# Kernel optimization log

Measured on AMD Instinct MI355X. Metric: run time of the kernel, lower is better.

The kernel has to match this reference:

```python
import jax, jax.numpy as jnp
import numpy as np

B, T, D, DL, E, H, K = 4, 2048, 1024, 128, 8, 4, 3
HD = DL // H


def setup_inputs() -> dict:
    key = jax.random.key(0)
    ks = jax.random.split(key, 12)
    s = jnp.float32(0.02)
    f = lambda k, shape: jax.random.normal(k, shape, dtype=jnp.float32)
    zeros = lambda n: jnp.zeros((n,), jnp.float32)
    ones = lambda n: jnp.ones((n,), jnp.float32)
    return {
        "x": f(ks[0], (B, T, D)),
        "w_down": f(ks[1], (E * DL, D)) * s,
        "expert_pos_embed": f(ks[2], (1, E, DL)) * s,
        "global_proj_w": f(ks[3], (DL, D)) * s,
        "global_proj_b": zeros(DL),
        "attn_in_w": f(ks[4], (3 * DL, DL)) * s,
        "attn_in_b": zeros(3 * DL),
        "attn_out_w": f(ks[5], (DL, DL)) * s,
        "attn_out_b": zeros(DL),
        "norm_w": ones(DL),
        "norm_b": zeros(DL),
        "rq1_w": f(ks[6], (DL, DL)) * s,
        "rq1_b": zeros(DL),
        "rq_ln_w": ones(DL),
        "rq_ln_b": zeros(DL),
        "rq2_w": f(ks[7], (DL, DL)) * s,
        "rq2_b": zeros(DL),
        "rk_w": f(ks[8], (DL, DL)) * s,
        "rk_b": zeros(DL),
        "w_up": f(ks[9], (E, DL, D)) * s,
    }


def _ln(x, w, b):
    m = jnp.mean(x, axis=-1, keepdims=True)
    v = jnp.mean((x - m) ** 2, axis=-1, keepdims=True)
    return (x - m) * jax.lax.rsqrt(v + 1e-5) * w + b


def _gelu(x):
    return jax.nn.gelu(x, approximate=False)  # torch nn.GELU() default is exact erf


def reference(x, w_down, expert_pos_embed, global_proj_w, global_proj_b,
              attn_in_w, attn_in_b, attn_out_w, attn_out_b, norm_w, norm_b,
              rq1_w, rq1_b, rq_ln_w, rq_ln_b, rq2_w, rq2_b, rk_w, rk_b, w_up):
    N = B * T
    xf = x.reshape(N, D)
    expert_feats = (xf @ w_down.T).reshape(N, E, DL)  # [N,E,DL]
    # global context, broadcast to every token as a length-1 query
    gctx = x.mean(axis=1) @ global_proj_w.T + global_proj_b  # [B,DL]
    gctx = jnp.broadcast_to(gctx[:, None, :], (B, T, DL)).reshape(N, 1, DL)
    # 9-token (1 global + E experts) self-attention round table
    seq = jnp.concatenate([gctx, expert_feats + expert_pos_embed], axis=1)  # [N,E+1,DL]
    qkv = seq @ attn_in_w.T + attn_in_b
    q, k, v = jnp.split(qkv, 3, axis=-1)
    split_heads = lambda t: t.reshape(N, E + 1, H, HD).transpose(0, 2, 1, 3)
    q, k, v = split_heads(q), split_heads(k), split_heads(v)
    attn = jax.nn.softmax(jnp.einsum('nhqd,nhkd->nhqk', q, k) / jnp.sqrt(jnp.float32(HD)), axis=-1)
    o = jnp.einsum('nhqk,nhkd->nhqd', attn, v).transpose(0, 2, 1, 3).reshape(N, E + 1, DL)
    o = o @ attn_out_w.T + attn_out_b
    seq2 = _ln(o + seq, norm_w, norm_b)
    refined = seq2[:, 1:, :]  # [N,E,DL]
    # routing: refined expert keys vs projected global query
    rq = _gelu(_ln(gctx[:, 0, :] @ rq1_w.T + rq1_b, rq_ln_w, rq_ln_b)) @ rq2_w.T + rq2_b  # [N,DL]
    rk = refined @ rk_w.T + rk_b  # [N,E,DL]
    logits = jnp.einsum('nd,ned->ne', rq, rk) / jnp.sqrt(jnp.float32(DL))
    probs = jax.nn.softmax(logits, axis=-1)
    tw, ti = jax.lax.top_k(probs, K)
    tw = tw / tw.sum(axis=-1, keepdims=True)
    # expert up-projection; computing all E then gathering top-k outputs is
    # mathematically identical to gathering w_up[indices] first, but avoids
    # materializing the [N,K,DL,D] duplicated weight tensor
    all_out = jnp.einsum('ned,edm->nem', _gelu(expert_feats), w_up)  # [N,E,D]
    sel_out = jnp.take_along_axis(all_out, ti[:, :, None], axis=1)  # [N,K,D]
    weighted = jnp.sum(sel_out * tw[:, :, None], axis=1)  # [N,D]
    # aux load-balance loss
    mean_prob = probs.mean(axis=0)
    one_hot = jnp.zeros((N, E), probs.dtype).at[jnp.arange(N)[:, None], ti].set(1.0)
    mean_load = one_hot.mean(axis=0)
    aux_loss = E * jnp.sum(mean_prob * mean_load)
    return weighted.reshape(B, T, D), aux_loss
```

## Files before the change

### kernel.cpp

```cpp
#include <hip/hip_runtime.h>
#include <hip/hip_bf16.h>
#include <math.h>

#define BB 4
#define TT 2048
#define DD 1024
#define DLb 128
#define EE 8
#define HH 4
#define KK 3
#define HDh 32
#define NN (BB*TT)
#define NPOS 9
#define NCH 16
#define CHL (TT/NCH)
#define SEQSTR (NPOS*DLb)
#define NSLICE 4
#define TSL (NN/NSLICE)

typedef __attribute__((ext_vector_type(8))) short short8;
typedef __attribute__((ext_vector_type(4))) float f32x4;
typedef __attribute__((ext_vector_type(8))) unsigned short ushort8;
typedef __attribute__((ext_vector_type(4))) unsigned short ushort4v;

#define GLL(gptr, lptr) \
    __builtin_amdgcn_global_load_lds((const __attribute__((address_space(1))) unsigned int*)(gptr), \
                                     (__attribute__((address_space(3))) unsigned int*)(lptr), 16, 0, 0)

__device__ __forceinline__ float gelu_exact(float v) {
    return 0.5f * v * (1.0f + erff(v * 0.70710678118654752440f));
}

__device__ __forceinline__ unsigned short f2bf(float x) {
    __hip_bfloat16 h = __float2bfloat16(x);
    return *reinterpret_cast<unsigned short*>(&h);
}

__device__ __forceinline__ float bf2f(unsigned short u) {
    return __uint_as_float(((unsigned int)u) << 16);
}

__device__ __forceinline__ float4 rec4(const unsigned short* h, const unsigned short* l) {
    ushort4v hv = *(const ushort4v*)h;
    ushort4v lv = *(const ushort4v*)l;
    float4 r;
    r.x = bf2f(hv[0]) + bf2f(lv[0]);
    r.y = bf2f(hv[1]) + bf2f(lv[1]);
    r.z = bf2f(hv[2]) + bf2f(lv[2]);
    r.w = bf2f(hv[3]) + bf2f(lv[3]);
    return r;
}

__device__ __forceinline__ void stage512(const unsigned short* __restrict__ G,
                                         size_t rowBase, int L, int k0,
                                         unsigned short* lds, int tid)
{
    int r = tid >> 2;
    int sl = tid & 3;
    int src = sl ^ ((r >> 1) & 3);
    GLL(&G[(rowBase + r) * (size_t)L + k0 + src * 8], lds + (tid >> 6) * 512);
}

__device__ __forceinline__ int fragoff(int row, int fq) {
    return row * 32 + ((fq ^ ((row >> 1) & 3)) << 3);
}

__global__ __launch_bounds__(256) void ksplit(const float* __restrict__ src,
                                              unsigned short* __restrict__ h,
                                              unsigned short* __restrict__ l, int n8)
{
    int i = blockIdx.x * 256 + threadIdx.x;
    if (i >= n8) return;
    size_t g = (size_t)i * 8;
    float4 a = *(const float4*)&src[g];
    float4 b = *(const float4*)&src[g + 4];
    float vv[8] = {a.x, a.y, a.z, a.w, b.x, b.y, b.z, b.w};
    ushort8 ho, lo;
    #pragma unroll
    for (int j = 0; j < 8; j++) {
        unsigned short hh = f2bf(vv[j]);
        float hf = bf2f(hh);
        ho[j] = hh;
        lo[j] = f2bf(vv[j] - hf);
    }
    *(ushort8*)&h[g] = ho;
    *(ushort8*)&l[g] = lo;
}

__global__ __launch_bounds__(256) void k1a(const float* __restrict__ x, float* __restrict__ partial,
                                           unsigned short* __restrict__ xh,
                                           unsigned short* __restrict__ xl) {
    int d = blockIdx.x * 256 + threadIdx.x;
    int b = blockIdx.y, c = blockIdx.z;
    size_t base = ((size_t)b * TT + (size_t)c * CHL) * DD + d;
    float s = 0.0f;
    for (int t = 0; t < CHL; t++) {
        size_t idx = base + (size_t)t * DD;
        float v = x[idx];
        s += v;
        unsigned short h = f2bf(v);
        xh[idx] = h;
        xl[idx] = f2bf(v - bf2f(h));
    }
    partial[(b * NCH + c) * DD + d] = s;
}

__global__ __launch_bounds__(256) void k1b(const float* __restrict__ partial, float* __restrict__ mean_x) {
    int d = blockIdx.x * 256 + threadIdx.x;
    int b = blockIdx.y;
    float s = 0.0f;
    for (int c = 0; c < NCH; c++) s += partial[(b * NCH + c) * DD + d];
    mean_x[b * DD + d] = s * (1.0f / TT);
}

__global__ __launch_bounds__(128) void k2_batch(
    const float* __restrict__ mean_x,
    const float* __restrict__ gpw, const float* __restrict__ gpb,
    const float* __restrict__ rq1w, const float* __restrict__ rq1b,
    const float* __restrict__ lnw, const float* __restrict__ lnb,
    const float* __restrict__ rq2w, const float* __restrict__ rq2b,
    const float* __restrict__ rkw, const float* __restrict__ rkb,
    float* __restrict__ gctx, float* __restrict__ uv, float* __restrict__ c0v)
{
    int b = blockIdx.x, d = threadIdx.x;
    __shared__ __attribute__((aligned(16))) float g[DLb];
    __shared__ __attribute__((aligned(16))) float t1[DLb];
    __shared__ __attribute__((aligned(16))) float act[DLb];
    __shared__ __attribute__((aligned(16))) float rqs[DLb];
    __shared__ float red[2];
    {
        const float4* wrow = (const float4*)(gpw + (size_t)d * DD);
        const float4* mx4  = (const float4*)(mean_x + (size_t)b * DD);
        float s = gpb[d];
        for (int k = 0; k < DD / 4; k++) {
            float4 w = wrow[k], m = mx4[k];
            s += w.x * m.x + w.y * m.y + w.z * m.z + w.w * m.w;
        }
        g[d] = s;
        gctx[b * DLb + d] = s;
    }
    __syncthreads();
    {
        float s = rq1b[d];
        for (int k = 0; k < DLb; k++) s += g[k] * rq1w[d * DLb + k];
        t1[d] = s;
    }
    __syncthreads();
    if (d == 0) {
        float m = 0.0f;
        for (int i = 0; i < DLb; i++) m += t1[i];
        m *= (1.0f / DLb);
        float v = 0.0f;
        for (int i = 0; i < DLb; i++) { float df = t1[i] - m; v += df * df; }
        v *= (1.0f / DLb);
        red[0] = m; red[1] = 1.0f / sqrtf(v + 1e-5f);
    }
    __syncthreads();
    {
        float xn = (t1[d] - red[0]) * red[1] * lnw[d] + lnb[d];
        act[d] = gelu_exact(xn);
    }
    __syncthreads();
    {
        float s = rq2b[d];
        for (int k = 0; k < DLb; k++) s += act[k] * rq2w[d * DLb + k];
        rqs[d] = s;
    }
    __syncthreads();
    {
        float u = 0.0f;
        for (int k = 0; k < DLb; k++) u += rqs[k] * rkw[(size_t)k * DLb + d];
        uv[b * DLb + d] = u;
    }
    if (d == 0) {
        float c0 = 0.0f;
        for (int k = 0; k < DLb; k++) c0 += rqs[k] * rkb[k];
        c0v[b] = c0;
    }
}

__global__ __launch_bounds__(256) void k2b(const float* __restrict__ gctx,
                                           unsigned short* __restrict__ seqh,
                                           unsigned short* __restrict__ seql) {
    int i = blockIdx.x * 256 + threadIdx.x;
    int n = i >> 7, d = i & 127;
    float v = gctx[(n >> 11) * DLb + d];
    unsigned short h = f2bf(v);
    seqh[(size_t)n * SEQSTR + d] = h;
    seql[(size_t)n * SEQSTR + d] = f2bf(v - bf2f(h));
}

__global__ __launch_bounds__(512, 4) void k3s(const unsigned short* __restrict__ XH,
                                              const unsigned short* __restrict__ XL,
                                              const unsigned short* __restrict__ WH,
                                              const unsigned short* __restrict__ WL,
                                              const float* __restrict__ pe,
                                              unsigned short* __restrict__ seqh,
                                              unsigned short* __restrict__ seql)
{
    __shared__ __attribute__((aligned(16))) unsigned short Ah[2][128 * 32];
    __shared__ __attribute__((aligned(16))) unsigned short Al[2][128 * 32];
    __shared__ __attribute__((aligned(16))) unsigned short Bh[2][128 * 32];
    __shared__ __attribute__((aligned(16))) unsigned short Bl[2][128 * 32];
    int tid = threadIdx.x;
    int lane = tid & 63, wave = tid >> 6;
    int wm = wave & 1, wn = wave >> 1;
    int b = blockIdx.y * 8 + blockIdx.x;
    int nbid = (b & 7) * 64 + (b >> 3);
    int row0 = (nbid >> 3) * 128, col0 = (nbid & 7) * 128;
    int fr = lane & 15, fq = lane >> 4;
    f32x4 acc[4][2];
    #pragma unroll
    for (int i = 0; i < 4; i++)
        #pragma unroll
        for (int j = 0; j < 2; j++) acc[i][j] = (f32x4)0.0f;

    for (int k0 = 0; k0 < DD; k0 += 64) {
        stage512(XH, row0, DD, k0,      Ah[0], tid);
        stage512(XH, row0, DD, k0 + 32, Ah[1], tid);
        stage512(XL, row0, DD, k0,      Al[0], tid);
        stage512(XL, row0, DD, k0 + 32, Al[1], tid);
        stage512(WH, col0, DD, k0,      Bh[0], tid);
        stage512(WH, col0, DD, k0 + 32, Bh[1], tid);
        stage512(WL, col0, DD, k0,      Bl[0], tid);
        stage512(WL, col0, DD, k0 + 32, Bl[1], tid);
        __syncthreads();
        #pragma unroll
        for (int ks = 0; ks < 2; ks++) {
            short8 ah[4], al4[4], bh[2], bl4[2];
            #pragma unroll
            for (int f = 0; f < 4; f++) {
                int ra = fragoff(wm * 64 + f * 16 + fr, fq);
                ah[f]  = *(const short8*)&Ah[ks][ra];
                al4[f] = *(const short8*)&Al[ks][ra];
            }
            #pragma unroll
            for (int g = 0; g < 2; g++) {
                int rb = fragoff(wn * 32 + g * 16 + fr, fq);
                bh[g]  = *(const short8*)&Bh[ks][rb];
                bl4[g] = *(const short8*)&Bl[ks][rb];
            }
            #pragma unroll
            for (int i = 0; i < 4; i++)
                #pragma unroll
                for (int j = 0; j < 2; j++) {
                    acc[i][j] = __builtin_amdgcn_mfma_f32_16x16x32_bf16(ah[i],  bh[j],  acc[i][j], 0, 0, 0);
                    acc[i][j] = __builtin_amdgcn_mfma_f32_16x16x32_bf16(ah[i],  bl4[j], acc[i][j], 0, 0, 0);
                    acc[i][j] = __builtin_amdgcn_mfma_f32_16x16x32_bf16(al4[i], bh[j],  acc[i][j], 0, 0, 0);
                }
        }
        __syncthreads();
    }
    #pragma unroll
    for (int j = 0; j < 2; j++) {
        int gc = col0 + wn * 32 + j * 16 + fr;
        float pv = pe[gc];
        #pragma unroll
        for (int i = 0; i < 4; i++) {
            #pragma unroll
            for (int r = 0; r < 4; r++) {
                int gr = row0 + wm * 64 + i * 16 + fq * 4 + r;
                float v = acc[i][j][r] + pv;
                unsigned short h = f2bf(v);
                size_t idx = (size_t)gr * SEQSTR + DLb + gc;
                seqh[idx] = h;
                seql[idx] = f2bf(v - bf2f(h));
            }
        }
    }
}

__global__ __launch_bounds__(512, 4) void k4as(const unsigned short* __restrict__ AHp,
                                               const unsigned short* __restrict__ ALp,
                                               const unsigned short* __restrict__ WHp,
                                               const unsigned short* __restrict__ WLp,
                                               const float* __restrict__ bias,
                                               float* __restrict__ C)
{
    __shared__ __attribute__((aligned(16))) unsigned short Ah[2][128 * 32];
    __shared__ __attribute__((aligned(16))) unsigned short Al[2][128 * 32];
    __shared__ __attribute__((aligned(16))) unsigned short Bh[2][128 * 32];
    __shared__ __attribute__((aligned(16))) unsigned short Bl[2][128 * 32];
    int tid = threadIdx.x;
    int lane = tid & 63, wave = tid >> 6;
    int wm = wave & 1, wn = wave >> 1;
    int b = blockIdx.y * 3 + blockIdx.x;
    int nbid = (b & 7) * 54 + (b >> 3);
    int row0 = (nbid / 3) * 128, col0 = (nbid % 3) * 128;
    int fr = lane & 15, fq = lane >> 4;
    f32x4 acc[4][2];
    #pragma unroll
    for (int i = 0; i < 4; i++)
        #pragma unroll
        for (int j = 0; j < 2; j++) acc[i][j] = (f32x4)0.0f;

    for (int k0 = 0; k0 < DLb; k0 += 64) {
        stage512(AHp, row0, DLb, k0,      Ah[0], tid);
        stage512(AHp, row0, DLb, k0 + 32, Ah[1], tid);
        stage512(ALp, row0, DLb, k0,      Al[0], tid);
        stage512(ALp, row0, DLb, k0 + 32, Al[1], tid);
        stage512(WHp, col0, DLb, k0,      Bh[0], tid);
        stage512(WHp, col0, DLb, k0 + 32, Bh[1], tid);
        stage512(WLp, col0, DLb, k0,      Bl[0], tid);
        stage512(WLp, col0, DLb, k0 + 32, Bl[1], tid);
        __syncthreads();
        #pragma unroll
        for (int ks = 0; ks < 2; ks++) {
            short8 ah[4], al4[4], bh[2], bl4[2];
            #pragma unroll
            for (int f = 0; f < 4; f++) {
                int ra = fragoff(wm * 64 + f * 16 + fr, fq);
                ah[f]  = *(const short8*)&Ah[ks][ra];
                al4[f] = *(const short8*)&Al[ks][ra];
            }
            #pragma unroll
            for (int g = 0; g < 2; g++) {
                int rb = fragoff(wn * 32 + g * 16 + fr, fq);
                bh[g]  = *(const short8*)&Bh[ks][rb];
                bl4[g] = *(const short8*)&Bl[ks][rb];
            }
            #pragma unroll
            for (int i = 0; i < 4; i++)
                #pragma unroll
                for (int j = 0; j < 2; j++) {
                    acc[i][j] = __builtin_amdgcn_mfma_f32_16x16x32_bf16(ah[i],  bh[j],  acc[i][j], 0, 0, 0);
                    acc[i][j] = __builtin_amdgcn_mfma_f32_16x16x32_bf16(ah[i],  bl4[j], acc[i][j], 0, 0, 0);
                    acc[i][j] = __builtin_amdgcn_mfma_f32_16x16x32_bf16(al4[i], bh[j],  acc[i][j], 0, 0, 0);
                }
        }
        __syncthreads();
    }
    #pragma unroll
    for (int j = 0; j < 2; j++) {
        int gc = col0 + wn * 32 + j * 16 + fr;
        float bv = bias[gc];
        #pragma unroll
        for (int i = 0; i < 4; i++) {
            #pragma unroll
            for (int r = 0; r < 4; r++) {
                int gr = row0 + wm * 64 + i * 16 + fq * 4 + r;
                C[(size_t)gr * 384 + gc] = acc[i][j][r] + bv;
            }
        }
    }
}

__global__ __launch_bounds__(256) void k4b(const float* __restrict__ qkv,
                                           float* __restrict__ og, int n0)
{
    int nl = blockIdx.x;
    int tid = threadIdx.x;
    __shared__ __attribute__((aligned(16))) float sq[NPOS][384];
    __shared__ float attnw[HH][NPOS][12];
    {
        const float4* src = (const float4*)(qkv + (size_t)nl * NPOS * 384);
        float4* dst = (float4*)&sq[0][0];
        for (int i = tid; i < NPOS * 384 / 4; i += 256) dst[i] = src[i];
    }
    __syncthreads();
    if (tid < HH * NPOS) {
        int h = tid / NPOS, i = tid % NPOS;
        float sc[NPOS];
        float mx = -1e30f;
        for (int j = 0; j < NPOS; j++) {
            float s = 0.0f;
            for (int d2 = 0; d2 < HDh; d2++)
                s += sq[i][h * HDh + d2] * sq[j][DLb + h * HDh + d2];
            s *= 0.17677669529663687f;
            sc[j] = s;
            mx = fmaxf(mx, s);
        }
        float se = 0.0f;
        for (int j = 0; j < NPOS; j++) { sc[j] = expf(sc[j] - mx); se += sc[j]; }
        float inv = 1.0f / se;
        for (int j = 0; j < NPOS; j++) attnw[h][i][j] = sc[j] * inv;
    }
    __syncthreads();
    #pragma unroll
    for (int it = 0; it < 4; it++) {
        int idx = it * 256 + tid;
        int p = 1 + (idx >> 7), d = idx & 127, h = d >> 5;
        float s = 0.0f;
        #pragma unroll
        for (int j = 0; j < NPOS; j++) s += attnw[h][p][j] * sq[j][2 * DLb + d];
        og[((size_t)(n0 + nl) * 8 + (p - 1)) * DLb + d] = s;
    }
}

__global__ __launch_bounds__(256) void k4cd(const float* __restrict__ A,
                                            const float* __restrict__ W,
                                            const float* __restrict__ bias,
                                            const unsigned short* __restrict__ seqh,
                                            const unsigned short* __restrict__ seql,
                                            const float* __restrict__ nw,
                                            const float* __restrict__ nb,
                                            const float* __restrict__ uv,
                                            const float* __restrict__ c0v,
                                            float* __restrict__ logits)
{
    __shared__ __attribute__((aligned(16))) float As[16][132];
    __shared__ __attribute__((aligned(16))) float Bs[16][132];
    __shared__ float redS[128][17];
    __shared__ float mstat[128][2];
    int tid = threadIdx.x;
    int tx = tid & 15, ty = tid >> 4;
    int row0 = blockIdx.y * 128;
    float acc[8][8] = {};
    for (int k0 = 0; k0 < DLb; k0 += 16) {
        #pragma unroll
        for (int i = 0; i < 2; i++) {
            int L = i * 256 + tid;
            int r = L >> 2, kq = (L & 3) * 4;
            float4 a4 = *(const float4*)&A[(size_t)(row0 + r) * DLb + k0 + kq];
            float4 b4 = *(const float4*)&W[(size_t)r * DLb + k0 + kq];
            As[kq + 0][r] = a4.x; As[kq + 1][r] = a4.y; As[kq + 2][r] = a4.z; As[kq + 3][r] = a4.w;
            Bs[kq + 0][r] = b4.x; Bs[kq + 1][r] = b4.y; Bs[kq + 2][r] = b4.z; Bs[kq + 3][r] = b4.w;
        }
        __syncthreads();
        #pragma unroll
        for (int kk = 0; kk < 16; kk++) {
            float4 a0 = *(const float4*)&As[kk][ty * 4];
            float4 a1 = *(const float4*)&As[kk][64 + ty * 4];
            float4 b0 = *(const float4*)&Bs[kk][tx * 4];
            float4 b1 = *(const float4*)&Bs[kk][64 + tx * 4];
            float ar[8] = {a0.x, a0.y, a0.z, a0.w, a1.x, a1.y, a1.z, a1.w};
            float bc[8] = {b0.x, b0.y, b0.z, b0.w, b1.x, b1.y, b1.z, b1.w};
            #pragma unroll
            for (int i = 0; i < 8; i++)
                #pragma unroll
                for (int j = 0; j < 8; j++)
                    acc[i][j] += ar[i] * bc[j];
        }
        __syncthreads();
    }
    int b = row0 >> 14;
    float4 bb0 = *(const float4*)&bias[tx * 4];
    float4 bb1 = *(const float4*)&bias[64 + tx * 4];
    #pragma unroll
    for (int i = 0; i < 8; i++) {
        int rl = (i < 4) ? (ty * 4 + i) : (64 + ty * 4 + (i - 4));
        int m = row0 + rl;
        size_t roff = (size_t)(m >> 3) * SEQSTR + (size_t)((m & 7) + 1) * DLb;
        float4 r0 = rec4(&seqh[roff + tx * 4], &seql[roff + tx * 4]);
        float4 r1 = rec4(&seqh[roff + 64 + tx * 4], &seql[roff + 64 + tx * 4]);
        acc[i][0] += bb0.x + r0.x; acc[i][1] += bb0.y + r0.y;
        acc[i][2] += bb0.z + r0.z; acc[i][3] += bb0.w + r0.w;
        acc[i][4] += bb1.x + r1.x; acc[i][5] += bb1.y + r1.y;
        acc[i][6] += bb1.z + r1.z; acc[i][7] += bb1.w + r1.w;
        float ps = 0.0f;
        #pragma unroll
        for (int j = 0; j < 8; j++) ps += acc[i][j];
        redS[rl][tx] = ps;
    }
    __syncthreads();
    if (tid < 128) {
        float s = 0.0f;
        #pragma unroll
        for (int t = 0; t < 16; t++) s += redS[tid][t];
        mstat[tid][0] = s * (1.0f / DLb);
    }
    __syncthreads();
    #pragma unroll
    for (int i = 0; i < 8; i++) {
        int rl = (i < 4) ? (ty * 4 + i) : (64 + ty * 4 + (i - 4));
        float m = mstat[rl][0];
        float pv = 0.0f;
        #pragma unroll
        for (int j = 0; j < 8; j++) { float df = acc[i][j] - m; pv += df * df; }
        redS[rl][tx] = pv;
    }
    __syncthreads();
    if (tid < 128) {
        float s = 0.0f;
        #pragma unroll
        for (int t = 0; t < 16; t++) s += redS[tid][t];
        mstat[tid][1] = 1.0f / sqrtf(s * (1.0f / DLb) + 1e-5f);
    }
    __syncthreads();
    const float* u = uv + b * DLb;
    float4 nw0 = *(const float4*)&nw[tx * 4];
    float4 nw1 = *(const float4*)&nw[64 + tx * 4];
    float4 nb0 = *(const float4*)&nb[tx * 4];
    float4 nb1 = *(const float4*)&nb[64 + tx * 4];
    float4 u0 = *(const float4*)&u[tx * 4];
    float4 u1 = *(const float4*)&u[64 + tx * 4];
    #pragma unroll
    for (int i = 0; i < 8; i++) {
        int rl = (i < 4) ? (ty * 4 + i) : (64 + ty * 4 + (i - 4));
        float m = mstat[rl][0], istd = mstat[rl][1];
        float ps;
        ps  = ((acc[i][0] - m) * istd * nw0.x + nb0.x) * u0.x;
        ps += ((acc[i][1] - m) * istd * nw0.y + nb0.y) * u0.y;
        ps += ((acc[i][2] - m) * istd * nw0.z + nb0.z) * u0.z;
        ps += ((acc[i][3] - m) * istd * nw0.w + nb0.w) * u0.w;
        ps += ((acc[i][4] - m) * istd * nw1.x + nb1.x) * u1.x;
        ps += ((acc[i][5] - m) * istd * nw1.y + nb1.y) * u1.y;
        ps += ((acc[i][6] - m) * istd * nw1.z + nb1.z) * u1.z;
        ps += ((acc[i][7] - m) * istd * nw1.w + nb1.w) * u1.w;
        redS[rl][tx] = ps;
    }
    __syncthreads();
    if (tid < 128) {
        float s = 0.0f;
        #pragma unroll
        for (int t = 0; t < 16; t++) s += redS[tid][t];
        logits[row0 + tid] = (s + c0v[b]) * 0.08838834764831845f;
    }
}

__global__ __launch_bounds__(256) void k4e(const float* __restrict__ logits,
                                           float* __restrict__ probs,
                                           float* __restrict__ wsel)
{
    int n = blockIdx.x * 256 + threadIdx.x;
    if (n >= NN) return;
    float lg[EE];
    float4 l0 = *(const float4*)&logits[(size_t)n * EE];
    float4 l1 = *(const float4*)&logits[(size_t)n * EE + 4];
    lg[0] = l0.x; lg[1] = l0.y; lg[2] = l0.z; lg[3] = l0.w;
    lg[4] = l1.x; lg[5] = l1.y; lg[6] = l1.z; lg[7] = l1.w;
    float mx = lg[0];
    #pragma unroll
    for (int e = 1; e < EE; e++) mx = fmaxf(mx, lg[e]);
    float pr[EE];
    float se = 0.0f;
    #pragma unroll
    for (int e = 0; e < EE; e++) { pr[e] = expf(lg[e] - mx); se += pr[e]; }
    float inv = 1.0f / se;
    #pragma unroll
    for (int e = 0; e < EE; e++) pr[e] *= inv;
    float4 p0, p1;
    p0.x = pr[0]; p0.y = pr[1]; p0.z = pr[2]; p0.w = pr[3];
    p1.x = pr[4]; p1.y = pr[5]; p1.z = pr[6]; p1.w = pr[7];
    *(float4*)&probs[(size_t)n * EE] = p0;
    *(float4*)&probs[(size_t)n * EE + 4] = p1;
    bool used[EE] = {};
    int sel[KK];
    float sw = 0.0f;
    for (int t = 0; t < KK; t++) {
        int bi = 0; float bv = -1e30f;
        for (int e = 0; e < EE; e++)
            if (!used[e] && pr[e] > bv) { bv = pr[e]; bi = e; }
        used[bi] = true; sel[t] = bi; sw += pr[bi];
    }
    float invsw = 1.0f / sw;
    float w8[EE];
    #pragma unroll
    for (int e = 0; e < EE; e++) w8[e] = 0.0f;
    for (int t = 0; t < KK; t++) w8[sel[t]] = pr[sel[t]] * invsw;
    float4 w0, w1;
    w0.x = w8[0]; w0.y = w8[1]; w0.z = w8[2]; w0.w = w8[3];
    w1.x = w8[4]; w1.y = w8[5]; w1.z = w8[6]; w1.w = w8[7];
    *(float4*)&wsel[(size_t)n * EE] = w0;
    *(float4*)&wsel[(size_t)n * EE + 4] = w1;
}

__global__ __launch_bounds__(256) void k5pre(const unsigned short* __restrict__ seqh,
                                             const unsigned short* __restrict__ seql,
                                             const float* __restrict__ pe,
                                             const float* __restrict__ wsel,
                                             unsigned short* __restrict__ abf)
{
    size_t g = ((size_t)blockIdx.x * 256 + threadIdx.x) * 8;
    int n = (int)(g >> 10), k0 = (int)(g & 1023);
    int e = k0 >> 7;
    float w = wsel[(size_t)n * EE + e];
    size_t soff = (size_t)n * SEQSTR + DLb + k0;
    ushort8 hv = *(const ushort8*)&seqh[soff];
    ushort8 lv = *(const ushort8*)&seql[soff];
    float4 p0 = *(const float4*)&pe[k0];
    float4 p1 = *(const float4*)&pe[k0 + 4];
    float pp[8] = {p0.x, p0.y, p0.z, p0.w, p1.x, p1.y, p1.z, p1.w};
    ushort8 o;
    #pragma unroll
    for (int i = 0; i < 8; i++) {
        float v = bf2f(hv[i]) + bf2f(lv[i]) - pp[i];
        o[i] = f2bf(w * gelu_exact(v));
    }
    *(ushort8*)&abf[g] = o;
}

__global__ __launch_bounds__(256) void k5t(const float* __restrict__ wup, unsigned short* __restrict__ wupT) {
    __shared__ float T[64][68];
    int tid = threadIdx.x;
    int k0 = blockIdx.x * 64, m0 = blockIdx.y * 64;
    #pragma unroll
    for (int i = 0; i < 4; i++) {
        int F = i * 256 + tid;
        int r = F >> 4, c4 = (F & 15) * 4;
        *(float4*)&T[r][c4] = *(const float4*)&wup[(size_t)(k0 + r) * DD + m0 + c4];
    }
    __syncthreads();
    #pragma unroll
    for (int i = 0; i < 2; i++) {
        int W = i * 256 + tid;
        int r = W >> 3, c8 = (W & 7) * 8;
        ushort8 o;
        #pragma unroll
        for (int j = 0; j < 8; j++) o[j] = f2bf(T[c8 + j][r]);
        *(ushort8*)&wupT[(size_t)(m0 + r) * DD + k0 + c8] = o;
    }
}

__global__ __launch_bounds__(512, 6) void k5_mfma(const unsigned short* __restrict__ A,
                                                  const unsigned short* __restrict__ B,
                                                  float* __restrict__ C)
{
    __shared__ __attribute__((aligned(16))) unsigned short As[2][128 * 32];
    __shared__ __attribute__((aligned(16))) unsigned short Bs[2][128 * 32];
    int tid = threadIdx.x;
    int lane = tid & 63, wave = tid >> 6;
    int wm = wave & 1, wn = wave >> 1;
    int b = blockIdx.y * 8 + blockIdx.x;
    int nbid = (b & 7) * 64 + (b >> 3);
    int row0 = (nbid >> 3) * 128, col0 = (nbid & 7) * 128;
    int fr = lane & 15, fq = lane >> 4;
    f32x4 acc[4][2];
    #pragma unroll
    for (int i = 0; i < 4; i++)
        #pragma unroll
        for (int j = 0; j < 2; j++) acc[i][j] = (f32x4)0.0f;

    for (int k0 = 0; k0 < DD; k0 += 64) {
        stage512(A, row0, DD, k0,      As[0], tid);
        stage512(A, row0, DD, k0 + 32, As[1], tid);
        stage512(B, col0, DD, k0,      Bs[0], tid);
        stage512(B, col0, DD, k0 + 32, Bs[1], tid);
        __syncthreads();
        #pragma unroll
        for (int ks = 0; ks < 2; ks++) {
            short8 af[4], bf[2];
            #pragma unroll
            for (int f = 0; f < 4; f++)
                af[f] = *(const short8*)&As[ks][fragoff(wm * 64 + f * 16 + fr, fq)];
            #pragma unroll
            for (int g = 0; g < 2; g++)
                bf[g] = *(const short8*)&Bs[ks][fragoff(wn * 32 + g * 16 + fr, fq)];
            #pragma unroll
            for (int i = 0; i < 4; i++)
                #pragma unroll
                for (int j = 0; j < 2; j++)
                    acc[i][j] = __builtin_amdgcn_mfma_f32_16x16x32_bf16(af[i], bf[j], acc[i][j], 0, 0, 0);
        }
        __syncthreads();
    }
    #pragma unroll
    for (int i = 0; i < 4; i++) {
        #pragma unroll
        for (int j = 0; j < 2; j++) {
            int gc = col0 + wn * 32 + j * 16 + fr;
            #pragma unroll
            for (int r = 0; r < 4; r++) {
                int gr = row0 + wm * 64 + i * 16 + fq * 4 + r;
                C[(size_t)gr * DD + gc] = acc[i][j][r];
            }
        }
    }
}

__global__ __launch_bounds__(256) void k6a(const float* __restrict__ probs,
                                           const float* __restrict__ wsel,
                                           float* __restrict__ part)
{
    int tid = threadIdx.x;
    int n = blockIdx.x * 256 + tid;
    float lp[EE], lc[EE];
    #pragma unroll
    for (int e = 0; e < EE; e++) {
        lp[e] = probs[(size_t)n * EE + e];
        lc[e] = (wsel[(size_t)n * EE + e] > 0.0f) ? 1.0f : 0.0f;
    }
    __shared__ float bp[256][EE];
    __shared__ float bc[256][EE];
    #pragma unroll
    for (int e = 0; e < EE; e++) { bp[tid][e] = lp[e]; bc[tid][e] = lc[e]; }
    __syncthreads();
    for (int s = 128; s > 0; s >>= 1) {
        if (tid < s) {
            #pragma unroll
            for (int e = 0; e < EE; e++) {
                bp[tid][e] += bp[tid + s][e];
                bc[tid][e] += bc[tid + s][e];
            }
        }
        __syncthreads();
    }
    if (tid < EE) {
        part[blockIdx.x * 16 + tid] = bp[0][tid];
        part[blockIdx.x * 16 + 8 + tid] = bc[0][tid];
    }
}

__global__ __launch_bounds__(64) void k6b(const float* __restrict__ part, float* __restrict__ out_aux) {
    int tid = threadIdx.x;
    __shared__ float sums[16];
    if (tid < 16) {
        float s = 0.0f;
        for (int b = 0; b < NN / 256; b++) s += part[b * 16 + tid];
        sums[tid] = s;
    }
    __syncthreads();
    if (tid == 0) {
        float a = 0.0f;
        for (int e = 0; e < EE; e++) a += (sums[e] / NN) * (sums[8 + e] / NN);
        out_aux[0] = EE * a;
    }
}

extern "C" void kernel_launch(void* const* d_in, const int* in_sizes, int n_in,
                              void* d_out, int out_size, void* d_ws, size_t ws_size,
                              hipStream_t stream) {
    const float* x     = (const float*)d_in[0];
    const float* wdown = (const float*)d_in[1];
    const float* pe    = (const float*)d_in[2];
    const float* gpw   = (const float*)d_in[3];
    const float* gpb   = (const float*)d_in[4];
    const float* aiw   = (const float*)d_in[5];
    const float* aib   = (const float*)d_in[6];
    const float* aow   = (const float*)d_in[7];
    const float* aob   = (const float*)d_in[8];
    const float* nw    = (const float*)d_in[9];
    const float* nb    = (const float*)d_in[10];
    const float* rq1w  = (const float*)d_in[11];
    const float* rq1b  = (const float*)d_in[12];
    const float* rqlnw = (const float*)d_in[13];
    const float* rqlnb = (const float*)d_in[14];
    const float* rq2w  = (const float*)d_in[15];
    const float* rq2b  = (const float*)d_in[16];
    const float* rkw   = (const float*)d_in[17];
    const float* rkb   = (const float*)d_in[18];
    const float* wup   = (const float*)d_in[19];

    float* out = (float*)d_out;

    unsigned short* seqh = (unsigned short*)d_ws;
    unsigned short* seql = seqh + (size_t)NN * SEQSTR;
    float* xregion = (float*)(seql + (size_t)NN * SEQSTR);
    unsigned short* xh = (unsigned short*)xregion;
    unsigned short* xl = xh + (size_t)NN * DD;
    float* o = xregion;
    unsigned short* abf = (unsigned short*)xregion;
    float* region = xregion + (size_t)NN * DD;
    float* qkvbuf = region;
    float* probs  = region + (size_t)65536 * 128;
    float* wsel   = probs + (size_t)NN * EE;
    float* logits = wsel + (size_t)NN * EE;
    float* partial= logits + (size_t)NN * EE;
    float* mean_x = partial + (size_t)BB * NCH * DD;
    float* gctx   = mean_x + (size_t)BB * DD;
    float* uv     = gctx + (size_t)BB * DLb;
    float* c0v    = uv + (size_t)BB * DLb;
    float* k6part = c0v + 64;
    unsigned short* wupT = (unsigned short*)(k6part + 512);
    unsigned short* wdh  = wupT + (size_t)DD * DD;
    unsigned short* wdl  = wdh + (size_t)DD * DD;
    unsigned short* aiwh = wdl + (size_t)DD * DD;
    unsigned short* aiwl = aiwh + (size_t)384 * DLb;

    hipLaunchKernelGGL(ksplit, dim3(DD * DD / 8 / 256), dim3(256), 0, stream, wdown, wdh, wdl, DD * DD / 8);
    hipLaunchKernelGGL(ksplit, dim3(384 * DLb / 8 / 256), dim3(256), 0, stream, aiw, aiwh, aiwl, 384 * DLb / 8);

    hipLaunchKernelGGL(k1a, dim3(DD / 256, BB, NCH), dim3(256), 0, stream, x, partial, xh, xl);
    hipLaunchKernelGGL(k1b, dim3(DD / 256, BB), dim3(256), 0, stream, partial, mean_x);
    hipLaunchKernelGGL(k2_batch, dim3(BB), dim3(DLb), 0, stream,
                       mean_x, gpw, gpb, rq1w, rq1b, rqlnw, rqlnb, rq2w, rq2b, rkw, rkb,
                       gctx, uv, c0v);
    hipLaunchKernelGGL(k2b, dim3(NN * DLb / 256), dim3(256), 0, stream, gctx, seqh, seql);
    hipLaunchKernelGGL(k3s, dim3((EE * DLb) / 128, NN / 128), dim3(512), 0, stream,
                       xh, xl, wdh, wdl, pe, seqh, seql);
    for (int s = 0; s < NSLICE; s++) {
        hipLaunchKernelGGL(k4as, dim3(3, TSL * NPOS / 128), dim3(512), 0, stream,
                           seqh + (size_t)s * TSL * SEQSTR, seql + (size_t)s * TSL * SEQSTR,
                           aiwh, aiwl, aib, qkvbuf);
        hipLaunchKernelGGL(k4b, dim3(TSL), dim3(256), 0, stream, qkvbuf, o, s * TSL);
    }
    hipLaunchKernelGGL(k4cd, dim3(1, NN * EE / 128), dim3(256), 0, stream,
                       o, aow, aob, seqh, seql, nw, nb, uv, c0v, logits);
    hipLaunchKernelGGL(k4e, dim3(NN / 256), dim3(256), 0, stream, logits, probs, wsel);
    hipLaunchKernelGGL(k5t, dim3(DD / 64, DD / 64), dim3(256), 0, stream, wup, wupT);
    hipLaunchKernelGGL(k5pre, dim3(NN * DD / (256 * 8)), dim3(256), 0, stream, seqh, seql, pe, wsel, abf);
    hipLaunchKernelGGL(k5_mfma, dim3(DD / 128, NN / 128), dim3(512), 0, stream, abf, wupT, out);
    hipLaunchKernelGGL(k6a, dim3(NN / 256), dim3(256), 0, stream, probs, wsel, k6part);
    hipLaunchKernelGGL(k6b, dim3(1), dim3(64), 0, stream, k6part, out + (size_t)NN * DD);
}
```

Before: 396.9 us.

## Fuse QKV projection GEMM with 9-token attention in one kernel

```diff
diff --git a/kernel.cpp b/kernel.cpp
--- a/kernel.cpp
+++ b/kernel.cpp
@@ -15,8 +15,6 @@
 #define NCH 16
 #define CHL (TT/NCH)
 #define SEQSTR (NPOS*DLb)
-#define NSLICE 4
-#define TSL (NN/NSLICE)
 
 typedef __attribute__((ext_vector_type(8))) short short8;
 typedef __attribute__((ext_vector_type(4))) float f32x4;
@@ -270,102 +268,101 @@
     }
 }
 
-__global__ __launch_bounds__(512, 4) void k4as(const unsigned short* __restrict__ AHp,
-                                               const unsigned short* __restrict__ ALp,
-                                               const unsigned short* __restrict__ WHp,
-                                               const unsigned short* __restrict__ WLp,
-                                               const float* __restrict__ bias,
-                                               float* __restrict__ C)
-{
-    __shared__ __attribute__((aligned(16))) unsigned short Ah[2][128 * 32];
-    __shared__ __attribute__((aligned(16))) unsigned short Al[2][128 * 32];
-    __shared__ __attribute__((aligned(16))) unsigned short Bh[2][128 * 32];
-    __shared__ __attribute__((aligned(16))) unsigned short Bl[2][128 * 32];
+__global__ __launch_bounds__(512, 2) void k4f(const unsigned short* __restrict__ SH,
+                                              const unsigned short* __restrict__ SL,
+                                              const unsigned short* __restrict__ WHp,
+                                              const unsigned short* __restrict__ WLp,
+                                              const float* __restrict__ bias,
+                                              float* __restrict__ og)
+{
+    __shared__ __attribute__((aligned(16))) float smemf[39968];
+    float* qbuf  = smemf;
+    float* kbuf  = smemf + 128 * 130;
+    float* attnw = smemf + 128 * 130 + 144 * 130;
+    float* vbuf  = smemf;
+    unsigned short* Ah = (unsigned short*)smemf;
+    unsigned short* Al = (unsigned short*)(smemf + 2304);
+
     int tid = threadIdx.x;
-    int lane = tid & 63, wave = tid >> 6;
-    int wm = wave & 1, wn = wave >> 1;
-    int b = blockIdx.y * 3 + blockIdx.x;
-    int nbid = (b & 7) * 54 + (b >> 3);
-    int row0 = (nbid / 3) * 128, col0 = (nbid % 3) * 128;
+    int lane = tid & 63, w = tid >> 6;
     int fr = lane & 15, fq = lane >> 4;
-    f32x4 acc[4][2];
-    #pragma unroll
-    for (int i = 0; i < 4; i++)
-        #pragma unroll
-        for (int j = 0; j < 2; j++) acc[i][j] = (f32x4)0.0f;
-
-    for (int k0 = 0; k0 < DLb; k0 += 64) {
-        stage512(AHp, row0, DLb, k0,      Ah[0], tid);
-        stage512(AHp, row0, DLb, k0 + 32, Ah[1], tid);
-        stage512(ALp, row0, DLb, k0,      Al[0], tid);
-        stage512(ALp, row0, DLb, k0 + 32, Al[1], tid);
-        stage512(WHp, col0, DLb, k0,      Bh[0], tid);
-        stage512(WHp, col0, DLb, k0 + 32, Bh[1], tid);
-        stage512(WLp, col0, DLb, k0,      Bl[0], tid);
-        stage512(WLp, col0, DLb, k0 + 32, Bl[1], tid);
+    int colBase = w * 48;
+    size_t rowBase = (size_t)blockIdx.x * 144;
+
+    f32x4 acc[9][3];
+    #pragma unroll
+    for (int i = 0; i < 9; i++)
+        #pragma unroll
+        for (int g = 0; g < 3; g++) acc[i][g] = (f32x4)0.0f;
+
+    for (int k0 = 0; k0 < DLb; k0 += 32) {
+        {
+            int r = tid >> 2, sl = tid & 3;
+            int src = sl ^ ((r >> 1) & 3);
+            GLL(&SH[(rowBase + r) * (size_t)DLb + k0 + src * 8], Ah + w * 512);
+            GLL(&SL[(rowBase + r) * (size_t)DLb + k0 + src * 8], Al + w * 512);
+            if (tid < 64) {
+                int r2 = 128 + (tid >> 2);
+                int src2 = (tid & 3) ^ ((r2 >> 1) & 3);
+                GLL(&SH[(rowBase + r2) * (size_t)DLb + k0 + src2 * 8], Ah + 4096);
+                GLL(&SL[(rowBase + r2) * (size_t)DLb + k0 + src2 * 8], Al + 4096);
+            }
+        }
         __syncthreads();
-        #pragma unroll
-        for (int ks = 0; ks < 2; ks++) {
-            short8 ah[4], al4[4], bh[2], bl4[2];
-            #pragma unroll
-            for (int f = 0; f < 4; f++) {
-                int ra = fragoff(wm * 64 + f * 16 + fr, fq);
-                ah[f]  = *(const short8*)&Ah[ks][ra];
-                al4[f] = *(const short8*)&Al[ks][ra];
+        short8 bh[3], bl[3];
+        #pragma unroll
+        for (int g = 0; g < 3; g++) {
+            int col = colBase + g * 16 + fr;
+            bh[g] = *(const short8*)&WHp[(size_t)col * DLb + k0 + fq * 8];
+            bl[g] = *(const short8*)&WLp[(size_t)col * DLb + k0 + fq * 8];
+        }
+        #pragma unroll
+        for (int i = 0; i < 9; i++) {
+            int ra = fragoff(i * 16 + fr, fq);
+            short8 ah  = *(const short8*)&Ah[ra];
+            short8 al4 = *(const short8*)&Al[ra];
+            #pragma unroll
+            for (int g = 0; g < 3; g++) {
+                acc[i][g] = __builtin_amdgcn_mfma_f32_16x16x32_bf16(ah,  bh[g], acc[i][g], 0, 0, 0);
+                acc[i][g] = __builtin_amdgcn_mfma_f32_16x16x32_bf16(ah,  bl[g], acc[i][g], 0, 0, 0);
+                acc[i][g] = __builtin_amdgcn_mfma_f32_16x16x32_bf16(al4, bh[g], acc[i][g], 0, 0, 0);
             }
-            #pragma unroll
-            for (int g = 0; g < 2; g++) {
-                int rb = fragoff(wn * 32 + g * 16 + fr, fq);
-                bh[g]  = *(const short8*)&Bh[ks][rb];
-                bl4[g] = *(const short8*)&Bl[ks][rb];
+        }
+        __syncthreads();
+    }
+
+    #pragma unroll
+    for (int g = 0; g < 3; g++) {
+        int cg = colBase + g * 16;
+        if (cg < 256) {
+            float bv = bias[cg + fr];
+            #pragma unroll
+            for (int i = 0; i < 9; i++) {
+                #pragma unroll
+                for (int rr = 0; rr < 4; rr++) {
+                    int lr = i * 16 + fq * 4 + rr;
+                    float v = acc[i][g][rr] + bv;
+                    if (cg < 128) {
+                        int t = lr / 9, p = lr - t * 9;
+                        if (p) qbuf[(t * 8 + p - 1) * 130 + cg + fr] = v;
+                    } else {
+                        kbuf[lr * 130 + (cg - 128) + fr] = v;
+                    }
+                }
             }
-            #pragma unroll
-            for (int i = 0; i < 4; i++)
-                #pragma unroll
-                for (int j = 0; j < 2; j++) {
-                    acc[i][j] = __builtin_amdgcn_mfma_f32_16x16x32_bf16(ah[i],  bh[j],  acc[i][j], 0, 0, 0);
-                    acc[i][j] = __builtin_amdgcn_mfma_f32_16x16x32_bf16(ah[i],  bl4[j], acc[i][j], 0, 0, 0);
-                    acc[i][j] = __builtin_amdgcn_mfma_f32_16x16x32_bf16(al4[i], bh[j],  acc[i][j], 0, 0, 0);
-                }
-        }
-        __syncthreads();
-    }
-    #pragma unroll
-    for (int j = 0; j < 2; j++) {
-        int gc = col0 + wn * 32 + j * 16 + fr;
-        float bv = bias[gc];
-        #pragma unroll
-        for (int i = 0; i < 4; i++) {
-            #pragma unroll
-            for (int r = 0; r < 4; r++) {
-                int gr = row0 + wm * 64 + i * 16 + fq * 4 + r;
-                C[(size_t)gr * 384 + gc] = acc[i][j][r] + bv;
-            }
-        }
-    }
-}
-
-__global__ __launch_bounds__(256) void k4b(const float* __restrict__ qkv,
-                                           float* __restrict__ og, int n0)
-{
-    int nl = blockIdx.x;
-    int tid = threadIdx.x;
-    __shared__ __attribute__((aligned(16))) float sq[NPOS][384];
-    __shared__ float attnw[HH][NPOS][12];
+        }
+    }
+    __syncthreads();
+
     {
-        const float4* src = (const float4*)(qkv + (size_t)nl * NPOS * 384);
-        float4* dst = (float4*)&sq[0][0];
-        for (int i = tid; i < NPOS * 384 / 4; i += 256) dst[i] = src[i];
-    }
-    __syncthreads();
-    if (tid < HH * NPOS) {
-        int h = tid / NPOS, i = tid % NPOS;
+        int t = tid >> 5, h = (tid >> 3) & 3, ii = 1 + (tid & 7);
+        const float* qrow = &qbuf[(t * 8 + ii - 1) * 130 + h * HDh];
         float sc[NPOS];
         float mx = -1e30f;
         for (int j = 0; j < NPOS; j++) {
+            const float* krow = &kbuf[(t * 9 + j) * 130 + h * HDh];
             float s = 0.0f;
-            for (int d2 = 0; d2 < HDh; d2++)
-                s += sq[i][h * HDh + d2] * sq[j][DLb + h * HDh + d2];
+            for (int d2 = 0; d2 < HDh; d2++) s += qrow[d2] * krow[d2];
             s *= 0.17677669529663687f;
             sc[j] = s;
             mx = fmaxf(mx, s);
@@ -373,17 +370,40 @@
         float se = 0.0f;
         for (int j = 0; j < NPOS; j++) { sc[j] = expf(sc[j] - mx); se += sc[j]; }
         float inv = 1.0f / se;
-        for (int j = 0; j < NPOS; j++) attnw[h][i][j] = sc[j] * inv;
-    }
-    __syncthreads();
-    #pragma unroll
-    for (int it = 0; it < 4; it++) {
-        int idx = it * 256 + tid;
-        int p = 1 + (idx >> 7), d = idx & 127, h = d >> 5;
-        float s = 0.0f;
-        #pragma unroll
-        for (int j = 0; j < NPOS; j++) s += attnw[h][p][j] * sq[j][2 * DLb + d];
-        og[((size_t)(n0 + nl) * 8 + (p - 1)) * DLb + d] = s;
+        for (int j = 0; j < NPOS; j++) attnw[((t * 4 + h) * 8 + (ii - 1)) * 9 + j] = sc[j] * inv;
+    }
+    __syncthreads();
+
+    #pragma unroll
+    for (int g = 0; g < 3; g++) {
+        int cg = colBase + g * 16;
+        if (cg >= 256) {
+            float bv = bias[cg + fr];
+            #pragma unroll
+            for (int i = 0; i < 9; i++) {
+                #pragma unroll
+                for (int rr = 0; rr < 4; rr++) {
+                    int lr = i * 16 + fq * 4 + rr;
+                    vbuf[lr * 130 + (cg - 256) + fr] = acc[i][g][rr] + bv;
+                }
+            }
+        }
+    }
+    __syncthreads();
+
+    {
+        int d = tid & 127, rb = tid >> 7;
+        int h = d >> 5;
+        #pragma unroll
+        for (int lr8 = 0; lr8 < 32; lr8++) {
+            int orow = rb * 32 + lr8;
+            int t = orow >> 3, pm1 = orow & 7;
+            const float* aw = &attnw[((t * 4 + h) * 8 + pm1) * 9];
+            float s = 0.0f;
+            #pragma unroll
+            for (int j = 0; j < NPOS; j++) s += aw[j] * vbuf[(t * 9 + j) * 130 + d];
+            og[((size_t)(blockIdx.x * 16 + t) * 8 + pm1) * DLb + d] = s;
+        }
     }
 }
 
@@ -741,7 +761,6 @@
     float* o = xregion;
     unsigned short* abf = (unsigned short*)xregion;
     float* region = xregion + (size_t)NN * DD;
-    float* qkvbuf = region;
     float* probs  = region + (size_t)65536 * 128;
     float* wsel   = probs + (size_t)NN * EE;
     float* logits = wsel + (size_t)NN * EE;
@@ -768,12 +787,8 @@
     hipLaunchKernelGGL(k2b, dim3(NN * DLb / 256), dim3(256), 0, stream, gctx, seqh, seql);
     hipLaunchKernelGGL(k3s, dim3((EE * DLb) / 128, NN / 128), dim3(512), 0, stream,
                        xh, xl, wdh, wdl, pe, seqh, seql);
-    for (int s = 0; s < NSLICE; s++) {
-        hipLaunchKernelGGL(k4as, dim3(3, TSL * NPOS / 128), dim3(512), 0, stream,
-                           seqh + (size_t)s * TSL * SEQSTR, seql + (size_t)s * TSL * SEQSTR,
-                           aiwh, aiwl, aib, qkvbuf);
-        hipLaunchKernelGGL(k4b, dim3(TSL), dim3(256), 0, stream, qkvbuf, o, s * TSL);
-    }
+    hipLaunchKernelGGL(k4f, dim3(NN / 16), dim3(512), 0, stream,
+                       seqh, seql, aiwh, aiwl, aib, o);
     hipLaunchKernelGGL(k4cd, dim3(1, NN * EE / 128), dim3(256), 0, stream,
                        o, aow, aob, seqh, seql, nw, nb, uv, c0v, logits);
     hipLaunchKernelGGL(k4e, dim3(NN / 256), dim3(256), 0, stream, logits, probs, wsel);
```

Measured after the change: 411.6 us. 3.7% more time.
